# Kernel optimization log

Hardware: AMD Instinct MI355X
Metric: run time of the kernel (lower is better)

## Reference

```python
import jax, jax.numpy as jnp
import numpy as np

H = 2880      # hidden_size
NH = 64       # num query heads
NKV = 8       # num kv heads
D = 64        # head_dim
G = NH // NKV # GQA group size
W = 128       # sliding window (keys per query, incl. self)
THETA = 150000.0
N = 1024      # tokens


def setup_inputs() -> dict:
    key = jax.random.key(0)
    k0, k1, k2, k3 = jax.random.split(key, 4)
    hidden_states = jax.random.normal(k0, (N, H), jnp.float32)
    Wqkv = jax.random.normal(k1, (H, (NH + 2 * NKV) * D), jnp.float32) * (H ** -0.5)
    Wo = jax.random.normal(k2, (NH * D, H), jnp.float32) * ((NH * D) ** -0.5)
    sinks = jax.random.normal(k3, (NH,), jnp.float32)
    positions = jnp.arange(N, dtype=jnp.int64)
    return {"hidden_states": hidden_states, "Wqkv": Wqkv, "Wo": Wo,
            "sinks": sinks, "positions": positions}


def _rope(x, pos):
    # NeoX-style rotary over full head_dim. x: [n, h, D], pos: [n]
    half = D // 2
    inv_freq = 1.0 / (THETA ** (jnp.arange(half, dtype=jnp.float32) / half))
    ang = pos[:, None].astype(jnp.float32) * inv_freq          # [n, half]
    cos = jnp.cos(ang)[:, None, :]
    sin = jnp.sin(ang)[:, None, :]
    x1, x2 = x[..., :half], x[..., half:]
    return jnp.concatenate([x1 * cos - x2 * sin, x2 * cos + x1 * sin], axis=-1)


def reference(hidden_states, Wqkv, Wo, sinks, positions):
    n = hidden_states.shape[0]
    qkv = hidden_states @ Wqkv
    q, k, v = jnp.split(qkv, [NH * D, NH * D + NKV * D], axis=-1)
    q = _rope(q.reshape(n, NH, D), positions)   # [n, NH, D]
    k = _rope(k.reshape(n, NKV, D), positions)  # [n, NKV, D]
    v = v.reshape(n, NKV, D)

    # Sliding-window key indices: query i attends keys j in [i-W+1, i]
    idx = positions[:, None] - (W - 1) + jnp.arange(W)[None, :]  # [n, W]
    valid = idx >= 0
    idx = jnp.clip(idx, 0, n - 1)
    k_win = k[idx]  # [n, W, NKV, D]
    v_win = v[idx]  # [n, W, NKV, D]

    qg = q.reshape(n, NKV, G, D)
    scores = jnp.einsum('nkgd,nwkd->nkgw', qg, k_win) * (D ** -0.5)
    scores = jnp.where(valid[:, None, None, :], scores, -jnp.inf)

    # Attention sinks: softmax over [scores, sink_logit]; sink gets no value.
    sink = sinks.reshape(NKV, G)                      # [NKV, G]
    m = jnp.maximum(scores.max(-1), sink[None])       # [n, NKV, G]
    p = jnp.exp(scores - m[..., None])                # [n, NKV, G, W]
    denom = p.sum(-1) + jnp.exp(sink[None] - m)       # [n, NKV, G]
    out = jnp.einsum('nkgw,nwkd->nkgd', p, v_win) / denom[..., None]
    return out.reshape(n, NH * D) @ Wo
```

## Files before the change

### kernel.cpp

```cpp
#include <hip/hip_runtime.h>
#include <hip/hip_bf16.h>

#define HDIM   2880
#define NH     64
#define NKV    8
#define DHEAD  64
#define GQ     (NH / NKV)
#define WIN    128
#define NTOK   1024
#define QKV_N  ((NH + 2 * NKV) * DHEAD)
#define QCOLS  (NH * DHEAD)
#define KOFF   QCOLS
#define VOFF   (QCOLS + NKV * DHEAD)
#define WO_PAD 3072
#define SK1    3
#define SK2    4

typedef __attribute__((ext_vector_type(8))) short short8;
typedef __attribute__((ext_vector_type(4))) float floatx4;

__device__ unsigned short g_Xb   [(size_t)NTOK  * HDIM];
__device__ unsigned short g_qkvb [(size_t)NTOK  * QKV_N];
__device__ unsigned short g_attn [(size_t)NTOK  * QCOLS];
__device__ unsigned short g_WqkvT[(size_t)QKV_N * HDIM];
__device__ unsigned short g_WoT  [(size_t)WO_PAD * QCOLS];
__device__ float          g_part1[(size_t)SK1 * NTOK * QKV_N];
__device__ float          g_part2[(size_t)SK2 * NTOK * WO_PAD];

__device__ __forceinline__ unsigned short f2b(float f) {
    __hip_bfloat16 h = __float2bfloat16(f);
    return *reinterpret_cast<unsigned short*>(&h);
}

__device__ __forceinline__ void gload_lds16(const unsigned short* g, unsigned short* l) {
    __builtin_amdgcn_global_load_lds(
        (const __attribute__((address_space(1))) unsigned int*)g,
        (__attribute__((address_space(3))) unsigned int*)l, 16, 0, 0);
}

#define T1_BLKS (45 * 80)
#define T2_BLKS (64 * 45)
#define CV_BLKS 2880

__global__ __launch_bounds__(256) void prep(
        const float* __restrict__ X, const float* __restrict__ Wqkv,
        const float* __restrict__ Wo, unsigned short* __restrict__ Xb,
        unsigned short* __restrict__ WqkvT, unsigned short* __restrict__ WoT) {
    __shared__ __align__(16) unsigned short T[64 * 72];
    int b = blockIdx.x, t = threadIdx.x;
    const float* in;
    unsigned short* out;
    int K, N, bk, bn;
    if (b < T1_BLKS) {
        in = Wqkv; out = WqkvT; K = HDIM; N = QKV_N;
        bk = b % 45; bn = b / 45;
    } else if (b < T1_BLKS + T2_BLKS) {
        int b2 = b - T1_BLKS;
        in = Wo; out = WoT; K = QCOLS; N = HDIM;
        bk = b2 % 64; bn = b2 / 64;
    } else {
        int id = (b - T1_BLKS - T2_BLKS) * 256 + t;
        float4 v = *(const float4*)(X + (size_t)id * 4);
        ushort4 o;
        o.x = f2b(v.x); o.y = f2b(v.y); o.z = f2b(v.z); o.w = f2b(v.w);
        *(ushort4*)(Xb + (size_t)id * 4) = o;
        return;
    }
    #pragma unroll
    for (int i = 0; i < 4; ++i) {
        int c = i * 256 + t;
        int r = c >> 4, cc = (c & 15) * 4;
        float4 v = *(const float4*)(in + (size_t)(bk * 64 + r) * N + bn * 64 + cc);
        T[r * 72 + cc + 0] = f2b(v.x);
        T[r * 72 + cc + 1] = f2b(v.y);
        T[r * 72 + cc + 2] = f2b(v.z);
        T[r * 72 + cc + 3] = f2b(v.w);
    }
    __syncthreads();
    #pragma unroll
    for (int i = 0; i < 2; ++i) {
        int c = i * 256 + t;
        int rn = c >> 3, kc = (c & 7) * 8;
        int4 vv;
        unsigned short* tp = (unsigned short*)&vv;
        #pragma unroll
        for (int j = 0; j < 8; ++j) tp[j] = T[(kc + j) * 72 + rn];
        *(int4*)(out + (size_t)(bn * 64 + rn) * K + bk * 64 + kc) = vv;
    }
}

__global__ __launch_bounds__(256) void gemm_sk(
        const unsigned short* __restrict__ A, const unsigned short* __restrict__ Bt,
        float* __restrict__ P, int K, int chunk, int ldc, size_t plane, int sk) {
    int sk8 = sk << 3;
    int xcd = blockIdx.x & 7;
    int idx = blockIdx.x >> 3;
    int grp = idx / sk8;
    int rem = idx - grp * sk8;
    int bn = xcd + (grp << 3);
    int bm = rem & 7;
    int z  = rem >> 3;

    int t = threadIdx.x, lane = t & 63, wid = t >> 6;
    int quad = lane >> 4, ml = lane & 15;
    int wm = wid >> 1, wn = wid & 1;
    __shared__ __align__(16) unsigned short As[128 * 64];
    __shared__ __align__(16) unsigned short Bs[128 * 64];
    floatx4 acc[4][4];
    #pragma unroll
    for (int i = 0; i < 4; ++i)
        #pragma unroll
        for (int j = 0; j < 4; ++j) acc[i][j] = (floatx4){0.f, 0.f, 0.f, 0.f};

    int srow = lane >> 3;
    int scol = (lane & 7) * 8;
    int base = z * chunk;
    const unsigned short* Ab = A  + (size_t)(bm * 128) * K + base;
    const unsigned short* Bb = Bt + (size_t)(bn * 128) * K + base;

    for (int k0 = 0; k0 < chunk; k0 += 64) {
        #pragma unroll
        for (int j = 0; j < 4; ++j) {
            int grp8 = wid * 4 + j;
            int r = grp8 * 8 + srow;
            gload_lds16(Ab + (size_t)r * K + k0 + scol, &As[grp8 * 512]);
            gload_lds16(Bb + (size_t)r * K + k0 + scol, &Bs[grp8 * 512]);
        }
        __syncthreads();
        #pragma unroll
        for (int kk = 0; kk < 64; kk += 32) {
            short8 af[4], bf[4];
            #pragma unroll
            for (int mt = 0; mt < 4; ++mt)
                af[mt] = *(const short8*)&As[(wm * 64 + mt * 16 + ml) * 64 + kk + quad * 8];
            #pragma unroll
            for (int nt = 0; nt < 4; ++nt)
                bf[nt] = *(const short8*)&Bs[(wn * 64 + nt * 16 + ml) * 64 + kk + quad * 8];
            #pragma unroll
            for (int mt = 0; mt < 4; ++mt)
                #pragma unroll
                for (int nt = 0; nt < 4; ++nt)
                    acc[mt][nt] = __builtin_amdgcn_mfma_f32_16x16x32_bf16(af[mt], bf[nt], acc[mt][nt], 0, 0, 0);
        }
        __syncthreads();
    }
    float* Cp = P + z * plane;
    #pragma unroll
    for (int mt = 0; mt < 4; ++mt)
        #pragma unroll
        for (int nt = 0; nt < 4; ++nt)
            #pragma unroll
            for (int r = 0; r < 4; ++r) {
                int row = bm * 128 + wm * 64 + mt * 16 + quad * 4 + r;
                int col = bn * 128 + wn * 64 + nt * 16 + ml;
                Cp[(size_t)row * ldc + col] = acc[mt][nt][r];
            }
}

#define QK_UNITS (NTOK * 72 * 8)
#define V_UNITS  (NTOK * 128)
__global__ __launch_bounds__(256) void reduce_rope(
        const float* __restrict__ P, unsigned short* __restrict__ qkvb) {
    int id = blockIdx.x * 256 + threadIdx.x;
    const size_t plane = (size_t)NTOK * QKV_N;
    if (id < QK_UNITS) {
        int n = id / 576;
        int rem = id - n * 576;
        int hh = rem >> 3, q8 = rem & 7;
        int c0 = (hh < NH) ? hh * 64 : KOFF + (hh - NH) * 64;
        size_t i1 = (size_t)n * QKV_N + c0 + q8 * 4;
        float4 a0 = *(const float4*)(P + i1);
        float4 a1 = *(const float4*)(P + plane + i1);
        float4 a2 = *(const float4*)(P + 2 * plane + i1);
        float4 b0 = *(const float4*)(P + i1 + 32);
        float4 b1 = *(const float4*)(P + plane + i1 + 32);
        float4 b2 = *(const float4*)(P + 2 * plane + i1 + 32);
        float x1[4] = {a0.x + a1.x + a2.x, a0.y + a1.y + a2.y,
                       a0.z + a1.z + a2.z, a0.w + a1.w + a2.w};
        float x2[4] = {b0.x + b1.x + b2.x, b0.y + b1.y + b2.y,
                       b0.z + b1.z + b2.z, b0.w + b1.w + b2.w};
        union { ushort4 v; unsigned short u[4]; } o1, o2;
        #pragma unroll
        for (int j = 0; j < 4; ++j) {
            int d = q8 * 4 + j;
            float inv = expf(-(float)d * 0.3724497053f);
            float ang = (float)n * inv;
            float s, c;
            sincosf(ang, &s, &c);
            o1.u[j] = f2b(x1[j] * c - x2[j] * s);
            o2.u[j] = f2b(x2[j] * c + x1[j] * s);
        }
        *(ushort4*)(qkvb + i1) = o1.v;
        *(ushort4*)(qkvb + i1 + 32) = o2.v;
    } else if (id < QK_UNITS + V_UNITS) {
        int vid = id - QK_UNITS;
        int n = vid >> 7, s8 = vid & 127;
        size_t i1 = (size_t)n * QKV_N + VOFF + s8 * 4;
        float4 a0 = *(const float4*)(P + i1);
        float4 a1 = *(const float4*)(P + plane + i1);
        float4 a2 = *(const float4*)(P + 2 * plane + i1);
        union { ushort4 v; unsigned short u[4]; } o;
        o.u[0] = f2b(a0.x + a1.x + a2.x);
        o.u[1] = f2b(a0.y + a1.y + a2.y);
        o.u[2] = f2b(a0.z + a1.z + a2.z);
        o.u[3] = f2b(a0.w + a1.w + a2.w);
        *(ushort4*)(qkvb + i1) = o.v;
    }
}

__global__ __launch_bounds__(256) void reduce_out(
        const float* __restrict__ P, float* __restrict__ out) {
    int id = blockIdx.x * 256 + threadIdx.x;
    if (id >= NTOK * (HDIM / 4)) return;
    int n = id / (HDIM / 4);
    int c = (id - n * (HDIM / 4)) * 4;
    const size_t plane = (size_t)NTOK * WO_PAD;
    size_t i = (size_t)n * WO_PAD + c;
    float4 a0 = *(const float4*)(P + i);
    float4 a1 = *(const float4*)(P + plane + i);
    float4 a2 = *(const float4*)(P + 2 * plane + i);
    float4 a3 = *(const float4*)(P + 3 * plane + i);
    float4 s;
    s.x = a0.x + a1.x + a2.x + a3.x;
    s.y = a0.y + a1.y + a2.y + a3.y;
    s.z = a0.z + a1.z + a2.z + a3.z;
    s.w = a0.w + a1.w + a2.w + a3.w;
    *(float4*)(out + (size_t)n * HDIM + c) = s;
}

#define TQ     16
#define WROWS  160
#define KS_LD  72
#define VT_LD  168
#define PS_LD  168

__global__ __launch_bounds__(256) void attn_mfma(
        const unsigned short* __restrict__ qkvb,
        const float* __restrict__ sinks,
        unsigned short* __restrict__ aout) {
    int t0 = blockIdx.x * TQ, kh = blockIdx.y;
    int t = threadIdx.x, lane = t & 63, wid = t >> 6;
    int quad = lane >> 4, ml = lane & 15;
    int wavebase = wid * 32;

    __shared__ __align__(16) unsigned short Ks[WROWS * KS_LD];
    __shared__ __align__(16) unsigned short Vt[DHEAD * VT_LD];
    __shared__ __align__(16) unsigned short Ps[4 * 16 * PS_LD];
    unsigned short* Psw = &Ps[wid * 16 * PS_LD];

    #pragma unroll
    for (int i = 0; i < 5; ++i) {
        int c = i * 256 + t;
        int w = c >> 3, d8 = (c & 7) * 8;
        int r = t0 - 127 + w;
        r = min(max(r, 0), NTOK - 1);
        *(int4*)&Ks[w * KS_LD + d8] =
            *(const int4*)(qkvb + (size_t)r * QKV_N + KOFF + kh * DHEAD + d8);
    }
    #pragma unroll
    for (int i = 0; i < 5; ++i) {
        int c = i * 256 + t;
        int w = c % 160, d8 = (c / 160) * 8;
        int r = t0 - 127 + w;
        r = min(max(r, 0), NTOK - 1);
        int4 vv = *(const int4*)(qkvb + (size_t)r * QKV_N + VOFF + kh * DHEAD + d8);
        const unsigned short* vp = (const unsigned short*)&vv;
        #pragma unroll
        for (int j = 0; j < 8; ++j) Vt[(d8 + j) * VT_LD + w] = vp[j];
    }
    __syncthreads();

    short8 qf[2][2];
    #pragma unroll
    for (int mt = 0; mt < 2; ++mt) {
        int m = wavebase + mt * 16 + ml;
        int tl = m & 15, g = m >> 4;
        const unsigned short* qp = qkvb + (size_t)(t0 + tl) * QKV_N + (kh * GQ + g) * DHEAD;
        #pragma unroll
        for (int kk = 0; kk < 2; ++kk)
            qf[mt][kk] = *(const short8*)(qp + kk * 32 + quad * 8);
    }

    floatx4 S[2][10];
    #pragma unroll
    for (int mt = 0; mt < 2; ++mt)
        #pragma unroll
        for (int nt = 0; nt < 10; ++nt) S[mt][nt] = (floatx4){0.f, 0.f, 0.f, 0.f};
    #pragma unroll
    for (int kk = 0; kk < 2; ++kk) {
        #pragma unroll
        for (int nt = 0; nt < 10; ++nt) {
            short8 kb = *(const short8*)&Ks[(nt * 16 + ml) * KS_LD + kk * 32 + quad * 8];
            #pragma unroll
            for (int mt = 0; mt < 2; ++mt)
                S[mt][nt] = __builtin_amdgcn_mfma_f32_16x16x32_bf16(qf[mt][kk], kb, S[mt][nt], 0, 0, 0);
        }
    }

    int wmin0 = 127 - t0;
    #pragma unroll
    for (int mt = 0; mt < 2; ++mt) {
        #pragma unroll
        for (int r = 0; r < 4; ++r) {
            int tl = (wavebase + mt * 16 + quad * 4 + r) & 15;
            int wlo = tl > wmin0 ? tl : wmin0;
            int whi = tl + 127;
            #pragma unroll
            for (int nt = 0; nt < 10; ++nt) {
                int w = nt * 16 + ml;
                float s = S[mt][nt][r] * 0.125f;
                S[mt][nt][r] = (w >= wlo && w <= whi) ? s : -INFINITY;
            }
        }
    }

    #pragma unroll
    for (int mt = 0; mt < 2; ++mt) {
        int g = (wavebase + mt * 16) >> 4;
        float sk = sinks[kh * GQ + g];
        #pragma unroll
        for (int r = 0; r < 4; ++r) {
            float rm = -INFINITY;
            #pragma unroll
            for (int nt = 0; nt < 10; ++nt) rm = fmaxf(rm, S[mt][nt][r]);
            #pragma unroll
            for (int off = 1; off < 16; off <<= 1) rm = fmaxf(rm, __shfl_xor(rm, off));
            rm = fmaxf(rm, sk);
            float sum = 0.f;
            #pragma unroll
            for (int nt = 0; nt < 10; ++nt) {
                float p = __expf(S[mt][nt][r] - rm);
                S[mt][nt][r] = p;
                sum += p;
            }
            #pragma unroll
            for (int off = 1; off < 16; off <<= 1) sum += __shfl_xor(sum, off);
            float inv = 1.f / (sum + __expf(sk - rm));
            #pragma unroll
            for (int nt = 0; nt < 10; ++nt) S[mt][nt][r] *= inv;
        }
    }

    #pragma unroll
    for (int mt = 0; mt < 2; ++mt) {
        #pragma unroll
        for (int r = 0; r < 4; ++r) {
            int lr = quad * 4 + r;
            #pragma unroll
            for (int nt = 0; nt < 10; ++nt)
                Psw[lr * PS_LD + nt * 16 + ml] = f2b(S[mt][nt][r]);
        }
        floatx4 O[4];
        #pragma unroll
        for (int j = 0; j < 4; ++j) O[j] = (floatx4){0.f, 0.f, 0.f, 0.f};
        #pragma unroll
        for (int ks = 0; ks < 5; ++ks) {
            short8 pf = *(const short8*)&Psw[ml * PS_LD + ks * 32 + quad * 8];
            #pragma unroll
            for (int nt = 0; nt < 4; ++nt) {
                short8 vf = *(const short8*)&Vt[(nt * 16 + ml) * VT_LD + ks * 32 + quad * 8];
                O[nt] = __builtin_amdgcn_mfma_f32_16x16x32_bf16(pf, vf, O[nt], 0, 0, 0);
            }
        }
        #pragma unroll
        for (int r = 0; r < 4; ++r) {
            int mm = wavebase + mt * 16 + quad * 4 + r;
            int tl = mm & 15, g = mm >> 4;
            unsigned short* op = aout + (size_t)(t0 + tl) * QCOLS + (kh * GQ + g) * DHEAD;
            #pragma unroll
            for (int nt = 0; nt < 4; ++nt)
                op[nt * 16 + ml] = f2b(O[nt][r]);
        }
    }
}

extern "C" void kernel_launch(void* const* d_in, const int* in_sizes, int n_in,
                              void* d_out, int out_size, void* d_ws, size_t ws_size,
                              hipStream_t stream) {
    const float* X     = (const float*)d_in[0];
    const float* Wqkv  = (const float*)d_in[1];
    const float* Wo    = (const float*)d_in[2];
    const float* sinks = (const float*)d_in[3];
    float* out = (float*)d_out;

    unsigned short *Xb, *qkvb, *attn, *WqkvT, *WoT;
    float *part1, *part2;
    hipGetSymbolAddress((void**)&Xb,    HIP_SYMBOL(g_Xb));
    hipGetSymbolAddress((void**)&qkvb,  HIP_SYMBOL(g_qkvb));
    hipGetSymbolAddress((void**)&attn,  HIP_SYMBOL(g_attn));
    hipGetSymbolAddress((void**)&WqkvT, HIP_SYMBOL(g_WqkvT));
    hipGetSymbolAddress((void**)&WoT,   HIP_SYMBOL(g_WoT));
    hipGetSymbolAddress((void**)&part1, HIP_SYMBOL(g_part1));
    hipGetSymbolAddress((void**)&part2, HIP_SYMBOL(g_part2));

    prep<<<T1_BLKS + T2_BLKS + CV_BLKS, 256, 0, stream>>>(X, Wqkv, Wo, Xb, WqkvT, WoT);

    gemm_sk<<<8 * 5 * 8 * SK1, 256, 0, stream>>>(
        Xb, WqkvT, part1, HDIM, HDIM / SK1, QKV_N, (size_t)NTOK * QKV_N, SK1);

    reduce_rope<<<(QK_UNITS + V_UNITS) / 256, 256, 0, stream>>>(part1, qkvb);

    attn_mfma<<<dim3(NTOK / TQ, NKV), 256, 0, stream>>>(qkvb, sinks, attn);

    gemm_sk<<<8 * 3 * 8 * SK2, 256, 0, stream>>>(
        attn, WoT, part2, QCOLS, QCOLS / SK2, WO_PAD, (size_t)NTOK * WO_PAD, SK2);

    reduce_out<<<(NTOK * (HDIM / 4) + 255) / 256, 256, 0, stream>>>(part2, out);
}
```

Baseline: 336.6 us.

## Store split-K partials in bf16 and raise split-K factors

Split-K partial sums in both GEMMs are now written as bf16 instead of fp32, which halves the partial-buffer traffic. The reduction kernels now read 8 elements per thread and accumulate in float. Split factors rise from 3/4 to 5/8 to expose more blocks. The XCD-aware block swizzle is dropped in favour of a plain 3D grid. Rounding each partial to bf16 adds numerical error. Dropping the swizzle may also hurt L2 locality across XCDs.

```diff
diff --git a/kernel.cpp b/kernel.cpp
--- a/kernel.cpp
+++ b/kernel.cpp
@@ -13,8 +13,8 @@
 #define KOFF   QCOLS
 #define VOFF   (QCOLS + NKV * DHEAD)
 #define WO_PAD 3072
-#define SK1    3
-#define SK2    4
+#define SK1    5
+#define SK2    8
 
 typedef __attribute__((ext_vector_type(8))) short short8;
 typedef __attribute__((ext_vector_type(4))) float floatx4;
@@ -24,12 +24,15 @@
 __device__ unsigned short g_attn [(size_t)NTOK  * QCOLS];
 __device__ unsigned short g_WqkvT[(size_t)QKV_N * HDIM];
 __device__ unsigned short g_WoT  [(size_t)WO_PAD * QCOLS];
-__device__ float          g_part1[(size_t)SK1 * NTOK * QKV_N];
-__device__ float          g_part2[(size_t)SK2 * NTOK * WO_PAD];
+__device__ unsigned short g_part1[(size_t)SK1 * NTOK * QKV_N];
+__device__ unsigned short g_part2[(size_t)SK2 * NTOK * WO_PAD];
 
 __device__ __forceinline__ unsigned short f2b(float f) {
     __hip_bfloat16 h = __float2bfloat16(f);
     return *reinterpret_cast<unsigned short*>(&h);
+}
+__device__ __forceinline__ float b2f(unsigned short u) {
+    union { unsigned int i; float f; } x; x.i = ((unsigned int)u) << 16; return x.f;
 }
 
 __device__ __forceinline__ void gload_lds16(const unsigned short* g, unsigned short* l) {
@@ -91,16 +94,8 @@
 
 __global__ __launch_bounds__(256) void gemm_sk(
         const unsigned short* __restrict__ A, const unsigned short* __restrict__ Bt,
-        float* __restrict__ P, int K, int chunk, int ldc, size_t plane, int sk) {
-    int sk8 = sk << 3;
-    int xcd = blockIdx.x & 7;
-    int idx = blockIdx.x >> 3;
-    int grp = idx / sk8;
-    int rem = idx - grp * sk8;
-    int bn = xcd + (grp << 3);
-    int bm = rem & 7;
-    int z  = rem >> 3;
-
+        unsigned short* __restrict__ P, int K, int chunk, int ldc, size_t plane) {
+    int bm = blockIdx.x, bn = blockIdx.y, z = blockIdx.z;
     int t = threadIdx.x, lane = t & 63, wid = t >> 6;
     int quad = lane >> 4, ml = lane & 15;
     int wm = wid >> 1, wn = wid & 1;
@@ -121,10 +116,10 @@
     for (int k0 = 0; k0 < chunk; k0 += 64) {
         #pragma unroll
         for (int j = 0; j < 4; ++j) {
-            int grp8 = wid * 4 + j;
-            int r = grp8 * 8 + srow;
-            gload_lds16(Ab + (size_t)r * K + k0 + scol, &As[grp8 * 512]);
-            gload_lds16(Bb + (size_t)r * K + k0 + scol, &Bs[grp8 * 512]);
+            int grp = wid * 4 + j;
+            int r = grp * 8 + srow;
+            gload_lds16(Ab + (size_t)r * K + k0 + scol, &As[grp * 512]);
+            gload_lds16(Bb + (size_t)r * K + k0 + scol, &Bs[grp * 512]);
         }
         __syncthreads();
         #pragma unroll
@@ -144,7 +139,7 @@
         }
         __syncthreads();
     }
-    float* Cp = P + z * plane;
+    unsigned short* Cp = P + z * plane;
     #pragma unroll
     for (int mt = 0; mt < 4; ++mt)
         #pragma unroll
@@ -153,36 +148,38 @@
             for (int r = 0; r < 4; ++r) {
                 int row = bm * 128 + wm * 64 + mt * 16 + quad * 4 + r;
                 int col = bn * 128 + wn * 64 + nt * 16 + ml;
-                Cp[(size_t)row * ldc + col] = acc[mt][nt][r];
+                Cp[(size_t)row * ldc + col] = f2b(acc[mt][nt][r]);
             }
 }
 
-#define QK_UNITS (NTOK * 72 * 8)
-#define V_UNITS  (NTOK * 128)
+#define QK8_UNITS (NTOK * 72 * 4)
+#define V8_UNITS  (NTOK * 64)
 __global__ __launch_bounds__(256) void reduce_rope(
-        const float* __restrict__ P, unsigned short* __restrict__ qkvb) {
+        const unsigned short* __restrict__ P, unsigned short* __restrict__ qkvb) {
     int id = blockIdx.x * 256 + threadIdx.x;
     const size_t plane = (size_t)NTOK * QKV_N;
-    if (id < QK_UNITS) {
-        int n = id / 576;
-        int rem = id - n * 576;
-        int hh = rem >> 3, q8 = rem & 7;
+    if (id < QK8_UNITS) {
+        int n = id / 288;
+        int rem = id - n * 288;
+        int hh = rem >> 2, o = rem & 3;
         int c0 = (hh < NH) ? hh * 64 : KOFF + (hh - NH) * 64;
-        size_t i1 = (size_t)n * QKV_N + c0 + q8 * 4;
-        float4 a0 = *(const float4*)(P + i1);
-        float4 a1 = *(const float4*)(P + plane + i1);
-        float4 a2 = *(const float4*)(P + 2 * plane + i1);
-        float4 b0 = *(const float4*)(P + i1 + 32);
-        float4 b1 = *(const float4*)(P + plane + i1 + 32);
-        float4 b2 = *(const float4*)(P + 2 * plane + i1 + 32);
-        float x1[4] = {a0.x + a1.x + a2.x, a0.y + a1.y + a2.y,
-                       a0.z + a1.z + a2.z, a0.w + a1.w + a2.w};
-        float x2[4] = {b0.x + b1.x + b2.x, b0.y + b1.y + b2.y,
-                       b0.z + b1.z + b2.z, b0.w + b1.w + b2.w};
-        union { ushort4 v; unsigned short u[4]; } o1, o2;
-        #pragma unroll
-        for (int j = 0; j < 4; ++j) {
-            int d = q8 * 4 + j;
+        size_t i1 = (size_t)n * QKV_N + c0 + o * 8;
+        float x1[8], x2[8];
+        #pragma unroll
+        for (int j = 0; j < 8; ++j) { x1[j] = 0.f; x2[j] = 0.f; }
+        #pragma unroll
+        for (int zz = 0; zz < SK1; ++zz) {
+            int4 a = *(const int4*)(P + zz * plane + i1);
+            int4 b = *(const int4*)(P + zz * plane + i1 + 32);
+            const unsigned short* ap = (const unsigned short*)&a;
+            const unsigned short* bp = (const unsigned short*)&b;
+            #pragma unroll
+            for (int j = 0; j < 8; ++j) { x1[j] += b2f(ap[j]); x2[j] += b2f(bp[j]); }
+        }
+        union { int4 v; unsigned short u[8]; } o1, o2;
+        #pragma unroll
+        for (int j = 0; j < 8; ++j) {
+            int d = o * 8 + j;
             float inv = expf(-(float)d * 0.3724497053f);
             float ang = (float)n * inv;
             float s, c;
@@ -190,42 +187,51 @@
             o1.u[j] = f2b(x1[j] * c - x2[j] * s);
             o2.u[j] = f2b(x2[j] * c + x1[j] * s);
         }
-        *(ushort4*)(qkvb + i1) = o1.v;
-        *(ushort4*)(qkvb + i1 + 32) = o2.v;
-    } else if (id < QK_UNITS + V_UNITS) {
-        int vid = id - QK_UNITS;
-        int n = vid >> 7, s8 = vid & 127;
-        size_t i1 = (size_t)n * QKV_N + VOFF + s8 * 4;
-        float4 a0 = *(const float4*)(P + i1);
-        float4 a1 = *(const float4*)(P + plane + i1);
-        float4 a2 = *(const float4*)(P + 2 * plane + i1);
-        union { ushort4 v; unsigned short u[4]; } o;
-        o.u[0] = f2b(a0.x + a1.x + a2.x);
-        o.u[1] = f2b(a0.y + a1.y + a2.y);
-        o.u[2] = f2b(a0.z + a1.z + a2.z);
-        o.u[3] = f2b(a0.w + a1.w + a2.w);
-        *(ushort4*)(qkvb + i1) = o.v;
+        *(int4*)(qkvb + i1) = o1.v;
+        *(int4*)(qkvb + i1 + 32) = o2.v;
+    } else if (id < QK8_UNITS + V8_UNITS) {
+        int vid = id - QK8_UNITS;
+        int n = vid >> 6, s = vid & 63;
+        size_t i1 = (size_t)n * QKV_N + VOFF + s * 8;
+        float v[8];
+        #pragma unroll
+        for (int j = 0; j < 8; ++j) v[j] = 0.f;
+        #pragma unroll
+        for (int zz = 0; zz < SK1; ++zz) {
+            int4 a = *(const int4*)(P + zz * plane + i1);
+            const unsigned short* ap = (const unsigned short*)&a;
+            #pragma unroll
+            for (int j = 0; j < 8; ++j) v[j] += b2f(ap[j]);
+        }
+        union { int4 w; unsigned short u[8]; } ov;
+        #pragma unroll
+        for (int j = 0; j < 8; ++j) ov.u[j] = f2b(v[j]);
+        *(int4*)(qkvb + i1) = ov.w;
     }
 }
 
 __global__ __launch_bounds__(256) void reduce_out(
-        const float* __restrict__ P, float* __restrict__ out) {
+        const unsigned short* __restrict__ P, float* __restrict__ out) {
     int id = blockIdx.x * 256 + threadIdx.x;
-    if (id >= NTOK * (HDIM / 4)) return;
-    int n = id / (HDIM / 4);
-    int c = (id - n * (HDIM / 4)) * 4;
+    if (id >= NTOK * 360) return;
+    int n = id / 360;
+    int c = (id - n * 360) * 8;
     const size_t plane = (size_t)NTOK * WO_PAD;
     size_t i = (size_t)n * WO_PAD + c;
-    float4 a0 = *(const float4*)(P + i);
-    float4 a1 = *(const float4*)(P + plane + i);
-    float4 a2 = *(const float4*)(P + 2 * plane + i);
-    float4 a3 = *(const float4*)(P + 3 * plane + i);
-    float4 s;
-    s.x = a0.x + a1.x + a2.x + a3.x;
-    s.y = a0.y + a1.y + a2.y + a3.y;
-    s.z = a0.z + a1.z + a2.z + a3.z;
-    s.w = a0.w + a1.w + a2.w + a3.w;
-    *(float4*)(out + (size_t)n * HDIM + c) = s;
+    float s[8];
+    #pragma unroll
+    for (int j = 0; j < 8; ++j) s[j] = 0.f;
+    #pragma unroll
+    for (int zz = 0; zz < SK2; ++zz) {
+        int4 a = *(const int4*)(P + zz * plane + i);
+        const unsigned short* ap = (const unsigned short*)&a;
+        #pragma unroll
+        for (int j = 0; j < 8; ++j) s[j] += b2f(ap[j]);
+    }
+    float4 lo = {s[0], s[1], s[2], s[3]};
+    float4 hi = {s[4], s[5], s[6], s[7]};
+    *(float4*)(out + (size_t)n * HDIM + c)     = lo;
+    *(float4*)(out + (size_t)n * HDIM + c + 4) = hi;
 }
 
 #define TQ     16
@@ -383,8 +389,7 @@
     const float* sinks = (const float*)d_in[3];
     float* out = (float*)d_out;
 
-    unsigned short *Xb, *qkvb, *attn, *WqkvT, *WoT;
-    float *part1, *part2;
+    unsigned short *Xb, *qkvb, *attn, *WqkvT, *WoT, *part1, *part2;
     hipGetSymbolAddress((void**)&Xb,    HIP_SYMBOL(g_Xb));
     hipGetSymbolAddress((void**)&qkvb,  HIP_SYMBOL(g_qkvb));
     hipGetSymbolAddress((void**)&attn,  HIP_SYMBOL(g_attn));
@@ -395,15 +400,15 @@
 
     prep<<<T1_BLKS + T2_BLKS + CV_BLKS, 256, 0, stream>>>(X, Wqkv, Wo, Xb, WqkvT, WoT);
 
-    gemm_sk<<<8 * 5 * 8 * SK1, 256, 0, stream>>>(
-        Xb, WqkvT, part1, HDIM, HDIM / SK1, QKV_N, (size_t)NTOK * QKV_N, SK1);
-
-    reduce_rope<<<(QK_UNITS + V_UNITS) / 256, 256, 0, stream>>>(part1, qkvb);
+    gemm_sk<<<dim3(NTOK / 128, QKV_N / 128, SK1), 256, 0, stream>>>(
+        Xb, WqkvT, part1, HDIM, HDIM / SK1, QKV_N, (size_t)NTOK * QKV_N);
+
+    reduce_rope<<<(QK8_UNITS + V8_UNITS) / 256, 256, 0, stream>>>(part1, qkvb);
 
     attn_mfma<<<dim3(NTOK / TQ, NKV), 256, 0, stream>>>(qkvb, sinks, attn);
 
-    gemm_sk<<<8 * 3 * 8 * SK2, 256, 0, stream>>>(
-        attn, WoT, part2, QCOLS, QCOLS / SK2, WO_PAD, (size_t)NTOK * WO_PAD, SK2);
-
-    reduce_out<<<(NTOK * (HDIM / 4) + 255) / 256, 256, 0, stream>>>(part2, out);
-}
+    gemm_sk<<<dim3(NTOK / 128, WO_PAD / 128, SK2), 256, 0, stream>>>(
+        attn, WoT, part2, QCOLS, QCOLS / SK2, WO_PAD, (size_t)NTOK * WO_PAD);
+
+    reduce_out<<<(NTOK * 360 + 255) / 256, 256, 0, stream>>>(part2, out);
+}
```

After: 335.3 us. Within noise of the previous version (-0.4%).
